# Kernel tuning notes

Hardware: AMD Instinct MI355X
Metric: run time of the kernel (lower is better)

The kernel has to match this reference:

```python
import jax, jax.numpy as jnp
import numpy as np

# Static dims (from init_kwargs / input_specs)
B, D, H, W, T, C = 1, 16, 32, 32, 4, 128
G, NH = 4, 8
HD = C // NH
NW = (D // G) * (H // G) * (W // G)   # windows per sample
N = G ** 3 * T                         # tokens per window (T-major ordering)
MLP_H = 4 * C
SCALE = 1.0 / float(np.sqrt(HD))
EPS = 1e-5


def _ln(x, g, b):
    m = x.mean(-1, keepdims=True)
    v = ((x - m) ** 2).mean(-1, keepdims=True)
    return (x - m) / jnp.sqrt(v + EPS) * g + b


def setup_inputs() -> dict:
    key = jax.random.key(0)
    ks = jax.random.split(key, 10)
    s = 0.02
    return {
        "x": jax.random.normal(ks[0], (B, D, H, W, T, C), jnp.float32),
        "norm1_g": jnp.ones((C,), jnp.float32),
        "norm1_b": jnp.zeros((C,), jnp.float32),
        "pos_embed": jax.random.normal(ks[1], (G, G, G, C), jnp.float32) * s,
        "time_embed": jax.random.normal(ks[2], (T, 1, 1, 1, C), jnp.float32) * s,
        "qkv_w": jax.random.normal(ks[3], (3 * C, C), jnp.float32) * s,
        "qkv_b": jnp.zeros((3 * C,), jnp.float32),
        "proj_w": jax.random.normal(ks[4], (C, C), jnp.float32) * s,
        "proj_b": jnp.zeros((C,), jnp.float32),
        "conv_w": jax.random.normal(ks[5], (C, 1, 3, 3, 3), jnp.float32) * s,  # depthwise
        "conv_b": jnp.zeros((C,), jnp.float32),
        "exln_g": jnp.ones((C,), jnp.float32),
        "exln_b": jnp.zeros((C,), jnp.float32),
        "norm2_g": jnp.ones((C,), jnp.float32),
        "norm2_b": jnp.zeros((C,), jnp.float32),
        "fc1_w": jax.random.normal(ks[6], (MLP_H, C), jnp.float32) * s,
        "fc1_b": jnp.zeros((MLP_H,), jnp.float32),
        "fc2_w": jax.random.normal(ks[7], (C, MLP_H), jnp.float32) * s,
        "fc2_b": jnp.zeros((C,), jnp.float32),
    }


def reference(x, norm1_g, norm1_b, pos_embed, time_embed, qkv_w, qkv_b,
              proj_w, proj_b, conv_w, conv_b, exln_g, exln_b,
              norm2_g, norm2_b, fc1_w, fc1_b, fc2_w, fc2_b):
    # --- window partition (lsda_flag=0, local SDA; dims divisible by G -> padding=0) ---
    xw = x.reshape(B, D // G, G, H // G, G, W // G, G, T, C)
    xw = xw.transpose(0, 1, 3, 5, 7, 2, 4, 6, 8)   # (B, Dg, Hg, Wg, T, G, G, G, C)
    xw = xw.reshape(B * NW, N, C)                   # token dim is T-major over (T,G,G,G)

    # --- pre-norm + window attention ---
    h = _ln(xw, norm1_g, norm1_b)
    h = h.reshape(B * NW, T, G, G, G, C)
    h = (h + pos_embed + time_embed).reshape(B * NW, N, C)  # learned spatial + temporal PE
    qkv = (h @ qkv_w.T + qkv_b).reshape(B * NW, N, 3, NH, HD).transpose(2, 0, 3, 1, 4)
    q, k, v = qkv[0] * SCALE, qkv[1], qkv[2]        # (B_, NH, N, HD)
    attn = jax.nn.softmax(jnp.einsum('bhnd,bhmd->bhnm', q, k), axis=-1)
    o = jnp.einsum('bhnm,bhmd->bhnd', attn, v).transpose(0, 2, 1, 3).reshape(B * NW, N, C)
    o = o @ proj_w.T + proj_b

    # --- window merge (inverse of partition) ---
    y = o.reshape(B, D // G, H // G, W // G, T, G, G, G, C)
    y = y.transpose(0, 1, 5, 2, 6, 3, 7, 4, 8).reshape(B, D, H, W, T, C)

    # --- depthwise 3x3x3 Conv3d over (D,H,W), T folded into batch, then LN ---
    xc = y.transpose(0, 4, 5, 1, 2, 3).reshape(B * T, C, D, H, W)
    xc = jax.lax.conv_general_dilated(
        xc, conv_w, window_strides=(1, 1, 1),
        padding=((1, 1), (1, 1), (1, 1)),
        feature_group_count=C,
        dimension_numbers=('NCDHW', 'OIDHW', 'NCDHW'))
    xc = xc + conv_b[None, :, None, None, None]
    y = xc.reshape(B, T, C, D, H, W).transpose(0, 3, 4, 5, 1, 2)
    y = _ln(y, exln_g, exln_b)

    # --- MLP with residual: x = mlp(norm2(x)) + x ---
    h2 = _ln(y, norm2_g, norm2_b)
    h2 = jax.nn.gelu(h2 @ fc1_w.T + fc1_b, approximate=False)
    h2 = h2 @ fc2_w.T + fc2_b
    return h2 + y
```

## Files before the change

### kernel.cpp

```cpp
#include <hip/hip_runtime.h>
#include <hip/hip_bf16.h>


typedef __attribute__((ext_vector_type(8))) short  s16x8;
typedef __attribute__((ext_vector_type(4))) short  s16x4;
typedef __attribute__((ext_vector_type(4))) float  f32x4;
typedef __attribute__((ext_vector_type(8))) _Float16 f16x8;
typedef __attribute__((ext_vector_type(4))) _Float16 f16x4;

#define CC    128
#define NWIN  256
#define TOKS  65536
#define SCALE 0.25f
#define LNEPS 1e-5f
#define PD 18
#define PH 34
#define PW 34
#define PSITES (PD*PH*PW)
#define Y1P_SHORTS ((size_t)PSITES*512)

__device__ __forceinline__ float b2f(short s) {
  union { unsigned u; float f; } c; c.u = ((unsigned)(unsigned short)s) << 16; return c.f;
}
__device__ __forceinline__ short f2b(float f) {
  __hip_bfloat16 h = __float2bfloat16(f);
  return *reinterpret_cast<short*>(&h);
}
__device__ __forceinline__ float fast_gelu(float x) {
  float u = 1.595769122f * x * fmaf(0.044715f, x*x, 1.0f);
  return x / (1.0f + __expf(-u));
}

__device__ __forceinline__ f32x4 mfma16x16x16_bf16(s16x4 a, s16x4 b, f32x4 c) {
#if __has_builtin(__builtin_amdgcn_mfma_f32_16x16x16_bf16)
  return __builtin_amdgcn_mfma_f32_16x16x16_bf16(a, b, c, 0, 0, 0);
#elif __has_builtin(__builtin_amdgcn_mfma_f32_16x16x16bf16_1k)
  return __builtin_amdgcn_mfma_f32_16x16x16bf16_1k(a, b, c, 0, 0, 0);
#else
  f32x4 d;
  asm("v_mfma_f32_16x16x16_bf16 %0, %1, %2, %3" : "=v"(d) : "v"(a), "v"(b), "v"(c));
  return d;
#endif
}

__device__ __forceinline__ void gload16(const short* g, short* l) {
  __builtin_amdgcn_global_load_lds(
      (const __attribute__((address_space(1))) void*)g,
      (__attribute__((address_space(3))) void*)l, 16, 0, 0);
}

__global__ void prep_kernel(const float* __restrict__ qkv_w, const float* __restrict__ proj_w,
                            const float* __restrict__ fc1_w, const float* __restrict__ fc2_w,
                            const float* __restrict__ conv_w,
                            __hip_bfloat16* wq, __hip_bfloat16* wp,
                            __hip_bfloat16* w1, __hip_bfloat16* w2, float* cwT) {
  int idx = blockIdx.x * 256 + threadIdx.x;
  if (idx < 49152) {
    wq[idx] = __float2bfloat16(qkv_w[idx]);
  } else if (idx < 65536) {
    wp[idx - 49152] = __float2bfloat16(proj_w[idx - 49152]);
  } else if (idx < 131072) {
    w1[idx - 65536] = __float2bfloat16(fc1_w[idx - 65536]);
  } else if (idx < 196608) {
    w2[idx - 131072] = __float2bfloat16(fc2_w[idx - 131072]);
  } else if (idx < 196608 + 27*128) {
    int j = idx - 196608;
    int tap = j >> 7, c = j & 127;
    cwT[tap*128 + c] = conv_w[c*27 + tap];
  }
}

__global__ __launch_bounds__(256) void border_zero_kernel(short* __restrict__ y1p) {
  int idx = blockIdx.x*256 + threadIdx.x;
  if (idx >= PSITES*64) return;
  int site = idx >> 6;
  int w = site % PW, hh = (site / PW) % PH, d = site / (PW*PH);
  if (d != 0 && d != PD-1 && hh != 0 && hh != PH-1 && w != 0 && w != PW-1) return;
  *(s16x8*)&y1p[(size_t)site*512 + (idx & 63)*8] = (s16x8)0;
}

__global__ __launch_bounds__(256) void ln1_pe_kernel(
    const float* __restrict__ x, const float* __restrict__ g, const float* __restrict__ b,
    const float* __restrict__ pos, const float* __restrict__ te,
    __hip_bfloat16* __restrict__ hb) {
  int wv = threadIdx.x >> 6, lane = threadIdx.x & 63;
  int tk = blockIdx.x * 4 + wv;
  int wid = tk >> 8, n = tk & 255;
  int t = n >> 6, gd = (n >> 4) & 3, gh = (n >> 2) & 3, gw = n & 3;
  int wd = wid >> 6, wh = (wid >> 3) & 7, ww = wid & 7;
  int d = wd*4 + gd, h = wh*4 + gh, w = ww*4 + gw;
  size_t xoff = ((size_t)((d*32 + h)*32 + w)*4 + t) * CC;
  float v0 = x[xoff + lane], v1 = x[xoff + lane + 64];
  float s = v0 + v1, sq = v0*v0 + v1*v1;
  for (int m = 32; m; m >>= 1) { s += __shfl_xor(s, m); sq += __shfl_xor(sq, m); }
  float mean = s * (1.f/128.f);
  float var  = sq * (1.f/128.f) - mean*mean;
  float rstd = rsqrtf(var + LNEPS);
  int pb = ((gd*4 + gh)*4 + gw) * CC, tb = t * CC;
  float h0 = (v0 - mean)*rstd*g[lane]    + b[lane]    + pos[pb + lane]    + te[tb + lane];
  float h1 = (v1 - mean)*rstd*g[lane+64] + b[lane+64] + pos[pb + lane+64] + te[tb + lane+64];
  hb[(size_t)tk*CC + lane]      = __float2bfloat16(h0);
  hb[(size_t)tk*CC + lane + 64] = __float2bfloat16(h1);
}

template <int MODE, int KK>
__global__ __launch_bounds__(256) void gemm_kernel(
    const short* __restrict__ Ag, const short* __restrict__ Wg,
    const float* __restrict__ bias,
    void* __restrict__ out0, const _Float16* __restrict__ resid) {
  __shared__ __align__(16) short As[128*64];
  __shared__ __align__(16) short Bs[128*64];
  const int tid = threadIdx.x;
  const int m0 = blockIdx.x * 128;
  const int n0 = blockIdx.y * 128;
  const int lane = tid & 63, wv = tid >> 6;
  const int wr = wv >> 1, wc = wv & 1;
  const int fr = lane & 15, kg = lane >> 4;

  f32x4 acc[4][4];
#pragma unroll
  for (int i = 0; i < 4; ++i)
#pragma unroll
    for (int j = 0; j < 4; ++j) acc[i][j] = (f32x4)0.f;

#pragma unroll
  for (int kc = 0; kc < KK; kc += 64) {
    __syncthreads();
#pragma unroll
    for (int i = 0; i < 4; ++i) {
      const int e = i*2048 + tid*8;
      const int row = e >> 6, col = e & 63;
      gload16(Ag + (size_t)(m0 + row)*KK + kc + col, &As[i*2048 + wv*512]);
      gload16(Wg + (size_t)(n0 + row)*KK + kc + col, &Bs[i*2048 + wv*512]);
    }
    __syncthreads();
#pragma unroll
    for (int ks = 0; ks < 2; ++ks) {
      s16x8 a[4], b[4];
#pragma unroll
      for (int i = 0; i < 4; ++i)
        a[i] = *(const s16x8*)&As[(wr*64 + i*16 + fr)*64 + ks*32 + kg*8];
#pragma unroll
      for (int j = 0; j < 4; ++j)
        b[j] = *(const s16x8*)&Bs[(wc*64 + j*16 + fr)*64 + ks*32 + kg*8];
#pragma unroll
      for (int i = 0; i < 4; ++i)
#pragma unroll
        for (int j = 0; j < 4; ++j)
          acc[i][j] = __builtin_amdgcn_mfma_f32_16x16x32_bf16(b[j], a[i], acc[i][j], 0, 0, 0);
    }
  }

  const int nbb = n0 + wc*64 + kg*4;
  f32x4 bj4[4];
#pragma unroll
  for (int j = 0; j < 4; ++j) bj4[j] = *(const f32x4*)&bias[nbb + j*16];

#pragma unroll
  for (int i = 0; i < 4; ++i) {
    const int m = m0 + wr*64 + i*16 + fr;
    if constexpr (MODE == 0) {
      short* qs = (short*)out0;
      const int sec = n0 >> 7;
      const float scl = (sec == 0) ? SCALE : 1.0f;
      const int wid = m >> 8, ntok = m & 255;
      const int rowbase = sec*8388608 + (wid*8)*4096 + ntok*16 + (nbb & 15);
#pragma unroll
      for (int j = 0; j < 4; ++j) {
        const int head = ((nbb + j*16) >> 4) & 7;
        f32x4 v = acc[i][j];
        s16x4 o;
        o[0] = f2b(fmaf(v[0], scl, bj4[j].x*scl));
        o[1] = f2b(fmaf(v[1], scl, bj4[j].y*scl));
        o[2] = f2b(fmaf(v[2], scl, bj4[j].z*scl));
        o[3] = f2b(fmaf(v[3], scl, bj4[j].w*scl));
        *(s16x4*)&qs[rowbase + head*4096] = o;
      }
    } else if constexpr (MODE == 1) {
      short* y1o = (short*)out0;
      const int wid = m >> 8, ntok = m & 255;
      const int t = ntok >> 6, gd = (ntok >> 4) & 3, gh = (ntok >> 2) & 3, gw = ntok & 3;
      const int wd = wid >> 6, wh = (wid >> 3) & 7, ww = wid & 7;
      const int sr = (((wd*4 + gd + 1)*PH + wh*4 + gh + 1)*PW + ww*4 + gw + 1)*4 + t;
      const int base = sr*CC + nbb;
#pragma unroll
      for (int j = 0; j < 4; ++j) {
        f32x4 v = acc[i][j];
        s16x4 o;
        o[0] = f2b(v[0] + bj4[j].x); o[1] = f2b(v[1] + bj4[j].y);
        o[2] = f2b(v[2] + bj4[j].z); o[3] = f2b(v[3] + bj4[j].w);
        *(s16x4*)&y1o[base + j*16] = o;
      }
    } else if constexpr (MODE == 2) {
      short* gp = (short*)out0;
      const int base = m*512 + nbb;
#pragma unroll
      for (int j = 0; j < 4; ++j) {
        f32x4 v = acc[i][j];
        s16x4 o;
        o[0] = f2b(fast_gelu(v[0] + bj4[j].x)); o[1] = f2b(fast_gelu(v[1] + bj4[j].y));
        o[2] = f2b(fast_gelu(v[2] + bj4[j].z)); o[3] = f2b(fast_gelu(v[3] + bj4[j].w));
        *(s16x4*)&gp[base + j*16] = o;
      }
    } else {
      float* outp = (float*)out0;
      const int base = m*CC + nbb;
#pragma unroll
      for (int j = 0; j < 4; ++j) {
        f32x4 v = acc[i][j];
        f16x4 rz = *(const f16x4*)&resid[base + j*16];
        f32x4 o;
        o.x = v[0] + bj4[j].x + (float)rz[0]; o.y = v[1] + bj4[j].y + (float)rz[1];
        o.z = v[2] + bj4[j].z + (float)rz[2]; o.w = v[3] + bj4[j].w + (float)rz[3];
        *(f32x4*)&outp[base + j*16] = o;
      }
    }
  }
}

#define KPAD 20
#define VPAD 264
__global__ __launch_bounds__(256) void attn_mfma_kernel(
    const __hip_bfloat16* __restrict__ qb, const __hip_bfloat16* __restrict__ kb,
    const __hip_bfloat16* __restrict__ vb, __hip_bfloat16* __restrict__ ob) {
  __shared__ __align__(16) short kL[256*KPAD];
  __shared__ __align__(16) short vT[16*VPAD];
  const int bh = blockIdx.x;
  const int wid = bh >> 3, head = bh & 7;
  const int tid = threadIdx.x;
  const short* kg = (const short*)kb + (size_t)bh*4096;
  const short* vg = (const short*)vb + (size_t)bh*4096;
  const short* qg = (const short*)qb + (size_t)bh*4096;
  {
    s16x8 a0 = *(const s16x8*)&kg[tid*16];
    s16x8 a1 = *(const s16x8*)&kg[tid*16 + 8];
    *(s16x8*)&kL[tid*KPAD]     = a0;
    *(s16x8*)&kL[tid*KPAD + 8] = a1;
    s16x8 b0 = *(const s16x8*)&vg[tid*16];
    s16x8 b1 = *(const s16x8*)&vg[tid*16 + 8];
#pragma unroll
    for (int d = 0; d < 8; ++d) {
      vT[d*VPAD + tid]     = b0[d];
      vT[(d+8)*VPAD + tid] = b1[d];
    }
  }
  __syncthreads();
  const int wv = tid >> 6, lane = tid & 63;
  const int fr = lane & 15, hi = lane >> 4;
  s16x4 kfrag[16], vfrag[16];
#pragma unroll
  for (int t = 0; t < 16; ++t) {
    kfrag[t] = *(const s16x4*)&kL[(t*16 + fr)*KPAD + hi*4];
    vfrag[t] = *(const s16x4*)&vT[fr*VPAD + t*16 + hi*4];
  }
  short* obs = (short*)ob;
  for (int qt = 0; qt < 4; ++qt) {
    const int q0 = wv*64 + qt*16;
    s16x4 qfrag = *(const s16x4*)&qg[(q0 + fr)*16 + hi*4];
    f32x4 st[16];
#pragma unroll
    for (int kt = 0; kt < 16; ++kt)
      st[kt] = mfma16x16x16_bf16(kfrag[kt], qfrag, (f32x4)0.f);
    float den = 0.f;
    f32x4 oacc = (f32x4)0.f;
#pragma unroll
    for (int kt = 0; kt < 16; ++kt) {
      float e0 = __expf(st[kt][0]), e1 = __expf(st[kt][1]);
      float e2 = __expf(st[kt][2]), e3 = __expf(st[kt][3]);
      den += (e0 + e1) + (e2 + e3);
      s16x4 pa;
      pa[0] = f2b(e0); pa[1] = f2b(e1); pa[2] = f2b(e2); pa[3] = f2b(e3);
      oacc = mfma16x16x16_bf16(vfrag[kt], pa, oacc);
    }
    den += __shfl_xor(den, 16);
    den += __shfl_xor(den, 32);
    float inv = 1.f / den;
    s16x4 ov;
    ov[0] = f2b(oacc[0]*inv); ov[1] = f2b(oacc[1]*inv);
    ov[2] = f2b(oacc[2]*inv); ov[3] = f2b(oacc[3]*inv);
    *(s16x4*)&obs[((size_t)wid*256 + q0 + fr)*CC + head*16 + hi*4] = ov;
  }
}

__global__ __launch_bounds__(256) void conv_ln_kernel(
    const __hip_bfloat16* __restrict__ y1p, const float* __restrict__ wT,
    const float* __restrict__ cb,
    const float* __restrict__ exg, const float* __restrict__ exb,
    const float* __restrict__ n2g, const float* __restrict__ n2b,
    _Float16* __restrict__ yb, __hip_bfloat16* __restrict__ h2) {
  const int tid = threadIdx.x;
  const int sp = blockIdx.x*16 + (tid >> 4);
  const int cbase = (tid & 15) * 8;
  const int w = sp & 31, h = (sp >> 5) & 31, d = sp >> 10;
  const int psite = ((d+1)*PH + (h+1))*PW + (w+1);
  const short* base = (const short*)y1p + (size_t)psite*512 + cbase;

  float acc[4][8];
  {
    f32x4 cb0 = *(const f32x4*)&cb[cbase];
    f32x4 cb1 = *(const f32x4*)&cb[cbase + 4];
#pragma unroll
    for (int t = 0; t < 4; ++t) {
      acc[t][0]=cb0.x; acc[t][1]=cb0.y; acc[t][2]=cb0.z; acc[t][3]=cb0.w;
      acc[t][4]=cb1.x; acc[t][5]=cb1.y; acc[t][6]=cb1.z; acc[t][7]=cb1.w;
    }
  }

#pragma unroll
  for (int dd = -1; dd <= 1; ++dd)
#pragma unroll
    for (int dh = -1; dh <= 1; ++dh)
#pragma unroll
      for (int dw = -1; dw <= 1; ++dw) {
        const int tap = ((dd+1)*3 + (dh+1))*3 + (dw+1);
        const int toff = ((dd*PH + dh)*PW + dw)*512;
        f32x4 w0 = *(const f32x4*)&wT[tap*CC + cbase];
        f32x4 w1 = *(const f32x4*)&wT[tap*CC + cbase + 4];
#pragma unroll
        for (int t = 0; t < 4; ++t) {
          s16x8 v = *(const s16x8*)(base + toff + t*CC);
          acc[t][0] = fmaf(b2f(v[0]), w0.x, acc[t][0]);
          acc[t][1] = fmaf(b2f(v[1]), w0.y, acc[t][1]);
          acc[t][2] = fmaf(b2f(v[2]), w0.z, acc[t][2]);
          acc[t][3] = fmaf(b2f(v[3]), w0.w, acc[t][3]);
          acc[t][4] = fmaf(b2f(v[4]), w1.x, acc[t][4]);
          acc[t][5] = fmaf(b2f(v[5]), w1.y, acc[t][5]);
          acc[t][6] = fmaf(b2f(v[6]), w1.z, acc[t][6]);
          acc[t][7] = fmaf(b2f(v[7]), w1.w, acc[t][7]);
        }
      }

  f32x4 eg0 = *(const f32x4*)&exg[cbase], eg1 = *(const f32x4*)&exg[cbase+4];
  f32x4 eb0 = *(const f32x4*)&exb[cbase], eb1 = *(const f32x4*)&exb[cbase+4];
  f32x4 ng0 = *(const f32x4*)&n2g[cbase], ng1 = *(const f32x4*)&n2g[cbase+4];
  f32x4 nb0 = *(const f32x4*)&n2b[cbase], nb1 = *(const f32x4*)&n2b[cbase+4];
  float eg[8] = {eg0.x,eg0.y,eg0.z,eg0.w,eg1.x,eg1.y,eg1.z,eg1.w};
  float eb[8] = {eb0.x,eb0.y,eb0.z,eb0.w,eb1.x,eb1.y,eb1.z,eb1.w};
  float ng[8] = {ng0.x,ng0.y,ng0.z,ng0.w,ng1.x,ng1.y,ng1.z,ng1.w};
  float nb[8] = {nb0.x,nb0.y,nb0.z,nb0.w,nb1.x,nb1.y,nb1.z,nb1.w};

#pragma unroll
  for (int t = 0; t < 4; ++t) {
    float s = 0.f, sq = 0.f;
#pragma unroll
    for (int c = 0; c < 8; ++c) { s += acc[t][c]; sq = fmaf(acc[t][c], acc[t][c], sq); }
#pragma unroll
    for (int m = 1; m <= 8; m <<= 1) { s += __shfl_xor(s, m); sq += __shfl_xor(sq, m); }
    float mean = s * (1.f/128.f);
    float var  = sq * (1.f/128.f) - mean*mean;
    float rstd = rsqrtf(var + LNEPS);
    float y[8];
    f16x8 yo;
#pragma unroll
    for (int c = 0; c < 8; ++c) {
      y[c] = (acc[t][c] - mean)*rstd*eg[c] + eb[c];
      yo[c] = (_Float16)y[c];
    }
    *(f16x8*)&yb[(size_t)(sp*4 + t)*CC + cbase] = yo;
    float s2 = 0.f, sq2 = 0.f;
#pragma unroll
    for (int c = 0; c < 8; ++c) { s2 += y[c]; sq2 = fmaf(y[c], y[c], sq2); }
#pragma unroll
    for (int m = 1; m <= 8; m <<= 1) { s2 += __shfl_xor(s2, m); sq2 += __shfl_xor(sq2, m); }
    float mean2 = s2 * (1.f/128.f);
    float var2  = sq2 * (1.f/128.f) - mean2*mean2;
    float rstd2 = rsqrtf(var2 + LNEPS);
    s16x8 ho;
#pragma unroll
    for (int c = 0; c < 8; ++c)
      ho[c] = f2b((y[c] - mean2)*rstd2*ng[c] + nb[c]);
    *(s16x8*)&((short*)h2)[(size_t)(sp*4 + t)*CC + cbase] = ho;
  }
}

extern "C" void kernel_launch(void* const* d_in, const int* in_sizes, int n_in,
                              void* d_out, int out_size, void* d_ws, size_t ws_size,
                              hipStream_t stream) {
  const float* x      = (const float*)d_in[0];
  const float* n1g    = (const float*)d_in[1];
  const float* n1b    = (const float*)d_in[2];
  const float* pos    = (const float*)d_in[3];
  const float* te     = (const float*)d_in[4];
  const float* qkv_w  = (const float*)d_in[5];
  const float* qkv_b  = (const float*)d_in[6];
  const float* proj_w = (const float*)d_in[7];
  const float* proj_b = (const float*)d_in[8];
  const float* conv_w = (const float*)d_in[9];
  const float* conv_b = (const float*)d_in[10];
  const float* exg    = (const float*)d_in[11];
  const float* exb    = (const float*)d_in[12];
  const float* n2g    = (const float*)d_in[13];
  const float* n2b    = (const float*)d_in[14];
  const float* fc1_w  = (const float*)d_in[15];
  const float* fc1_b  = (const float*)d_in[16];
  const float* fc2_w  = (const float*)d_in[17];
  const float* fc2_b  = (const float*)d_in[18];

  char* wsb = (char*)d_ws;
  __hip_bfloat16* wq  = (__hip_bfloat16*)(wsb);
  __hip_bfloat16* wp  = (__hip_bfloat16*)(wsb + 98304);
  __hip_bfloat16* w1  = (__hip_bfloat16*)(wsb + 131072);
  __hip_bfloat16* w2  = (__hip_bfloat16*)(wsb + 262144);
  float*          cwT = (float*)(wsb + 393216);

  const size_t A_OFF = (size_t)1 << 20;
  const size_t B_OFF = A_OFF + ((size_t)16 << 20);
  const size_t C_OFF = B_OFF + ((size_t)48 << 20);

  __hip_bfloat16* hbuf = (__hip_bfloat16*)(wsb + A_OFF);
  __hip_bfloat16* obuf = (__hip_bfloat16*)(wsb + A_OFF);
  __hip_bfloat16* h2in = (__hip_bfloat16*)(wsb + A_OFF);
  __hip_bfloat16* qkvb = (__hip_bfloat16*)(wsb + B_OFF);
  __hip_bfloat16* qb   = qkvb;
  __hip_bfloat16* kb   = qkvb + 8388608;
  __hip_bfloat16* vb   = qkvb + 16777216;
  __hip_bfloat16* y1p  = (__hip_bfloat16*)(wsb + B_OFF);
  _Float16* yb = (_Float16*)(wsb + B_OFF + ((size_t)24 << 20));
  __hip_bfloat16* gbuf = (__hip_bfloat16*)(wsb + C_OFF);

  prep_kernel<<<782, 256, 0, stream>>>(qkv_w, proj_w, fc1_w, fc2_w, conv_w,
                                       wq, wp, w1, w2, cwT);
  ln1_pe_kernel<<<TOKS/4, 256, 0, stream>>>(x, n1g, n1b, pos, te, hbuf);
  gemm_kernel<0, 128><<<dim3(TOKS/128, 3), 256, 0, stream>>>(
      (const short*)hbuf, (const short*)wq, qkv_b, (void*)qkvb, nullptr);
  attn_mfma_kernel<<<NWIN*8, 256, 0, stream>>>(qb, kb, vb, obuf);
  border_zero_kernel<<<(PSITES*64 + 255)/256, 256, 0, stream>>>((short*)y1p);
  gemm_kernel<1, 128><<<dim3(TOKS/128, 1), 256, 0, stream>>>(
      (const short*)obuf, (const short*)wp, proj_b, (void*)y1p, nullptr);
  conv_ln_kernel<<<16384/16, 256, 0, stream>>>(y1p, cwT, conv_b,
      exg, exb, n2g, n2b, yb, h2in);
  gemm_kernel<2, 128><<<dim3(TOKS/128, 4), 256, 0, stream>>>(
      (const short*)h2in, (const short*)w1, fc1_b, (void*)gbuf, nullptr);
  gemm_kernel<3, 512><<<dim3(TOKS/128, 1), 256, 0, stream>>>(
      (const short*)gbuf, (const short*)w2, fc2_b, (void*)d_out, yb);
}
```

Before: 173.6 us.

## Fuse fc1+GELU+fc2 MLP into a single kernel keeping hidden activations in registers

```diff
diff --git a/kernel.cpp b/kernel.cpp
--- a/kernel.cpp
+++ b/kernel.cpp
@@ -176,7 +176,7 @@
         o[3] = f2b(fmaf(v[3], scl, bj4[j].w*scl));
         *(s16x4*)&qs[rowbase + head*4096] = o;
       }
-    } else if constexpr (MODE == 1) {
+    } else {
       short* y1o = (short*)out0;
       const int wid = m >> 8, ntok = m & 255;
       const int t = ntok >> 6, gd = (ntok >> 4) & 3, gh = (ntok >> 2) & 3, gw = ntok & 3;
@@ -191,29 +191,106 @@
         o[2] = f2b(v[2] + bj4[j].z); o[3] = f2b(v[3] + bj4[j].w);
         *(s16x4*)&y1o[base + j*16] = o;
       }
-    } else if constexpr (MODE == 2) {
-      short* gp = (short*)out0;
-      const int base = m*512 + nbb;
-#pragma unroll
-      for (int j = 0; j < 4; ++j) {
-        f32x4 v = acc[i][j];
-        s16x4 o;
-        o[0] = f2b(fast_gelu(v[0] + bj4[j].x)); o[1] = f2b(fast_gelu(v[1] + bj4[j].y));
-        o[2] = f2b(fast_gelu(v[2] + bj4[j].z)); o[3] = f2b(fast_gelu(v[3] + bj4[j].w));
-        *(s16x4*)&gp[base + j*16] = o;
+    }
+  }
+}
+
+__global__ __launch_bounds__(256) void mlp_kernel(
+    const short* __restrict__ h2, const short* __restrict__ w1,
+    const short* __restrict__ w2, const float* __restrict__ b1,
+    const float* __restrict__ b2, const _Float16* __restrict__ resid,
+    float* __restrict__ out) {
+  __shared__ __align__(16) short As[128*128];
+  __shared__ __align__(16) short Ws[128*128];
+  const int tid = threadIdx.x;
+  const int m0 = blockIdx.x * 128;
+  const int lane = tid & 63, wv = tid >> 6;
+  const int fr = lane & 15, kg = lane >> 4;
+
+#pragma unroll
+  for (int i = 0; i < 8; ++i) {
+    const int e = i*2048 + tid*8;
+    const int row = e >> 7, col = e & 127;
+    gload16(h2 + (size_t)(m0 + row)*128 + col, &As[i*2048 + wv*512]);
+  }
+
+  f32x4 acc2[2][8];
+#pragma unroll
+  for (int i = 0; i < 2; ++i)
+#pragma unroll
+    for (int c = 0; c < 8; ++c) acc2[i][c] = (f32x4)0.f;
+
+#pragma unroll
+  for (int s = 0; s < 4; ++s) {
+    __syncthreads();
+#pragma unroll
+    for (int i = 0; i < 8; ++i) {
+      const int e = i*2048 + tid*8;
+      const int row = e >> 7, col = e & 127;
+      gload16(w1 + (size_t)(s*128 + row)*128 + col, &Ws[i*2048 + wv*512]);
+    }
+    __syncthreads();
+
+    f32x4 acc1[2][8];
+#pragma unroll
+    for (int i = 0; i < 2; ++i)
+#pragma unroll
+      for (int j = 0; j < 8; ++j) acc1[i][j] = (f32x4)0.f;
+#pragma unroll
+    for (int ks = 0; ks < 4; ++ks) {
+      s16x8 a[2], b[8];
+#pragma unroll
+      for (int i = 0; i < 2; ++i)
+        a[i] = *(const s16x8*)&As[(wv*32 + i*16 + fr)*128 + ks*32 + kg*8];
+#pragma unroll
+      for (int j = 0; j < 8; ++j)
+        b[j] = *(const s16x8*)&Ws[(j*16 + fr)*128 + ks*32 + kg*8];
+#pragma unroll
+      for (int i = 0; i < 2; ++i)
+#pragma unroll
+        for (int j = 0; j < 8; ++j)
+          acc1[i][j] = __builtin_amdgcn_mfma_f32_16x16x32_bf16(b[j], a[i], acc1[i][j], 0, 0, 0);
+    }
+
+#pragma unroll
+    for (int j = 0; j < 8; ++j) {
+      f32x4 b1v = *(const f32x4*)&b1[s*128 + j*16 + kg*4];
+      s16x4 pa[2];
+#pragma unroll
+      for (int i = 0; i < 2; ++i) {
+        f32x4 v = acc1[i][j];
+        pa[i][0] = f2b(fast_gelu(v[0] + b1v.x));
+        pa[i][1] = f2b(fast_gelu(v[1] + b1v.y));
+        pa[i][2] = f2b(fast_gelu(v[2] + b1v.z));
+        pa[i][3] = f2b(fast_gelu(v[3] + b1v.w));
       }
-    } else {
-      float* outp = (float*)out0;
-      const int base = m*CC + nbb;
-#pragma unroll
-      for (int j = 0; j < 4; ++j) {
-        f32x4 v = acc[i][j];
-        f16x4 rz = *(const f16x4*)&resid[base + j*16];
-        f32x4 o;
-        o.x = v[0] + bj4[j].x + (float)rz[0]; o.y = v[1] + bj4[j].y + (float)rz[1];
-        o.z = v[2] + bj4[j].z + (float)rz[2]; o.w = v[3] + bj4[j].w + (float)rz[3];
-        *(f32x4*)&outp[base + j*16] = o;
+      const int koff = s*128 + j*16 + kg*4;
+#pragma unroll
+      for (int ct = 0; ct < 8; ++ct) {
+        s16x4 wf = *(const s16x4*)&w2[(ct*16 + fr)*512 + koff];
+#pragma unroll
+        for (int i = 0; i < 2; ++i)
+          acc2[i][ct] = mfma16x16x16_bf16(wf, pa[i], acc2[i][ct]);
       }
+    }
+  }
+
+#pragma unroll
+  for (int i = 0; i < 2; ++i) {
+    const int m = m0 + wv*32 + i*16 + fr;
+#pragma unroll
+    for (int ct = 0; ct < 8; ++ct) {
+      const int c = ct*16 + kg*4;
+      const int base = m*CC + c;
+      f32x4 b2v = *(const f32x4*)&b2[c];
+      f16x4 rz = *(const f16x4*)&resid[base];
+      f32x4 v = acc2[i][ct];
+      f32x4 o;
+      o.x = v[0] + b2v.x + (float)rz[0];
+      o.y = v[1] + b2v.y + (float)rz[1];
+      o.z = v[2] + b2v.z + (float)rz[2];
+      o.w = v[3] + b2v.w + (float)rz[3];
+      *(f32x4*)&out[base] = o;
     }
   }
 }
@@ -405,7 +482,6 @@
 
   const size_t A_OFF = (size_t)1 << 20;
   const size_t B_OFF = A_OFF + ((size_t)16 << 20);
-  const size_t C_OFF = B_OFF + ((size_t)48 << 20);
 
   __hip_bfloat16* hbuf = (__hip_bfloat16*)(wsb + A_OFF);
   __hip_bfloat16* obuf = (__hip_bfloat16*)(wsb + A_OFF);
@@ -416,7 +492,6 @@
   __hip_bfloat16* vb   = qkvb + 16777216;
   __hip_bfloat16* y1p  = (__hip_bfloat16*)(wsb + B_OFF);
   _Float16* yb = (_Float16*)(wsb + B_OFF + ((size_t)24 << 20));
-  __hip_bfloat16* gbuf = (__hip_bfloat16*)(wsb + C_OFF);
 
   prep_kernel<<<782, 256, 0, stream>>>(qkv_w, proj_w, fc1_w, fc2_w, conv_w,
                                        wq, wp, w1, w2, cwT);
@@ -429,8 +504,7 @@
       (const short*)obuf, (const short*)wp, proj_b, (void*)y1p, nullptr);
   conv_ln_kernel<<<16384/16, 256, 0, stream>>>(y1p, cwT, conv_b,
       exg, exb, n2g, n2b, yb, h2in);
-  gemm_kernel<2, 128><<<dim3(TOKS/128, 4), 256, 0, stream>>>(
-      (const short*)h2in, (const short*)w1, fc1_b, (void*)gbuf, nullptr);
-  gemm_kernel<3, 512><<<dim3(TOKS/128, 1), 256, 0, stream>>>(
-      (const short*)gbuf, (const short*)w2, fc2_b, (void*)d_out, yb);
-}
+  mlp_kernel<<<TOKS/128, 256, 0, stream>>>(
+      (const short*)h2in, (const short*)w1, (const short*)w2,
+      fc1_b, fc2_b, yb, (float*)d_out);
+}
```

New measurement: 228.2 us. 31.5% more time.
